# Kernel optimization log

Hardware: AMD Instinct MI355X
Metric: run time of the kernel (lower is better)

The kernel has to match this reference:

```python
import jax, jax.numpy as jnp
import numpy as np


def setup_inputs() -> dict:
    key = jax.random.key(0)
    # coeffs_tensor: stacked/padded wavelet coefficients [B, F, T]
    coeffs = jax.random.normal(key, (16, 256, 8192), dtype=jnp.float32)
    return {"coeffs": coeffs}


def reference(coeffs) -> jnp.ndarray:
    B, F, T = coeffs.shape
    # torch.angle on a real tensor -> 0 for x>=0, pi for x<0; jnp.angle matches.
    phase = jnp.angle(coeffs)
    inst_freq = jnp.diff(phase, axis=-1)
    inst_freq = jnp.pad(inst_freq, ((0, 0), (0, 0), (0, 1)))  # F.pad(..., (0,1))
    freq_adjusted = jnp.clip(inst_freq, -1.0, 1.0)  # [B,F,T]
    # k = (f + freq_adjusted).long(); .long() truncates toward zero, as does astype(int32)
    f_idx = jnp.arange(F, dtype=coeffs.dtype)[None, :, None]
    k = jnp.clip((f_idx + freq_adjusted).astype(jnp.int32), 0, F - 1)  # [B,F,T]
    # Fused scatter-add over all (b, f, t): sst[b, k[b,f,t], t] += coeffs[b, f, t]
    b_idx = jnp.arange(B)[:, None, None]
    t_idx = jnp.arange(T)[None, None, :]
    sst = jnp.zeros_like(coeffs).at[b_idx, k, t_idx].add(coeffs)
    return sst
```

## Files before the change

kernel.cpp:

```cpp
#include <hip/hip_runtime.h>

#define BB 16
#define FF 256
#define TT 8192
#define F_CHUNK 64
#define THREADS 256

__device__ __forceinline__ int sgn_bit(float x) {
    return (int)(__float_as_uint(x) >> 31);
}

__global__ __launch_bounds__(THREADS) void sst_kernel(const float* __restrict__ in,
                                                      float* __restrict__ out) {
    const int t   = blockIdx.x * (THREADS * 4) + threadIdx.x * 4;
    const int fs  = blockIdx.y * F_CHUNK;
    const int b   = blockIdx.z;
    const int lane = threadIdx.x & 63;

    const float* src = in  + (size_t)b * FF * TT + t;
    float*       dst = out + (size_t)b * FF * TT + t;

    const bool tail = (t + 4 >= TT);

    float4 vprev, vcur, vnext;
    int4   aprev, acur, anext;

    auto load_row = [&](int f, float4& v, int4& a) {
        v = *reinterpret_cast<const float4*>(src + (size_t)f * TT);
        float nxt = __shfl_down(v.x, 1, 64);
        if (lane == 63) {
            nxt = tail ? 0.0f : src[(size_t)f * TT + 4];
        }
        const int s0 = sgn_bit(v.x), s1 = sgn_bit(v.y), s2 = sgn_bit(v.z),
                  s3 = sgn_bit(v.w), s4 = sgn_bit(nxt);
        a.x = s1 - s0;
        a.y = s2 - s1;
        a.z = s3 - s2;
        a.w = tail ? 0 : (s4 - s3);
    };

    if (fs == 0) {
        aprev = make_int4(9, 9, 9, 9);
        vprev = make_float4(0.f, 0.f, 0.f, 0.f);
    } else {
        load_row(fs - 1, vprev, aprev);
    }
    load_row(fs, vcur, acur);

    #pragma unroll 4
    for (int g = fs; g < fs + F_CHUNK; ++g) {
        if (g + 1 < FF) {
            load_row(g + 1, vnext, anext);
        } else {
            anext = make_int4(9, 9, 9, 9);
            vnext = make_float4(0.f, 0.f, 0.f, 0.f);
        }

        const bool isFirst = (g == 0);
        const bool isLast  = (g == FF - 1);

        float4 r;
        {
            const bool bc = (acur.x == 0) || (isFirst && acur.x < 0) || (isLast && acur.x > 0);
            r.x = ((aprev.x == 1) ? vprev.x : 0.f) + (bc ? vcur.x : 0.f)
                + ((anext.x == -1) ? vnext.x : 0.f);
        }
        {
            const bool bc = (acur.y == 0) || (isFirst && acur.y < 0) || (isLast && acur.y > 0);
            r.y = ((aprev.y == 1) ? vprev.y : 0.f) + (bc ? vcur.y : 0.f)
                + ((anext.y == -1) ? vnext.y : 0.f);
        }
        {
            const bool bc = (acur.z == 0) || (isFirst && acur.z < 0) || (isLast && acur.z > 0);
            r.z = ((aprev.z == 1) ? vprev.z : 0.f) + (bc ? vcur.z : 0.f)
                + ((anext.z == -1) ? vnext.z : 0.f);
        }
        {
            const bool bc = (acur.w == 0) || (isFirst && acur.w < 0) || (isLast && acur.w > 0);
            r.w = ((aprev.w == 1) ? vprev.w : 0.f) + (bc ? vcur.w : 0.f)
                + ((anext.w == -1) ? vnext.w : 0.f);
        }

        *reinterpret_cast<float4*>(dst + (size_t)g * TT) = r;

        vprev = vcur; aprev = acur;
        vcur  = vnext; acur  = anext;
    }
}

extern "C" void kernel_launch(void* const* d_in, const int* in_sizes, int n_in,
                              void* d_out, int out_size, void* d_ws, size_t ws_size,
                              hipStream_t stream) {
    const float* in  = (const float*)d_in[0];
    float*       out = (float*)d_out;
    dim3 grid(TT / (THREADS * 4), FF / F_CHUNK, BB);
    sst_kernel<<<grid, THREADS, 0, stream>>>(in, out);
}
```

Before: 272.4 us.

## Prefetch rows two ahead and shrink frequency chunk for more blocks

Splits the row load into a raw-load step and a separate sign-difference step, so the load for row g+2 is issued before row g+1's data is consumed. This gives a software-pipelined prefetch that hides global memory latency. F_CHUNK also drops from 64 to 16, which quadruples the grid size for more parallelism and fully unrolls the loop. The cost is more halo rows loaded per block (about 18 rows read per 16 written) and higher register pressure.

```diff
diff --git a/kernel.cpp b/kernel.cpp
--- a/kernel.cpp
+++ b/kernel.cpp
@@ -3,18 +3,20 @@
 #define BB 16
 #define FF 256
 #define TT 8192
-#define F_CHUNK 64
+#define F_CHUNK 16
 #define THREADS 256
 
 __device__ __forceinline__ int sgn_bit(float x) {
     return (int)(__float_as_uint(x) >> 31);
 }
 
+struct Raw { float4 v; float e; };
+
 __global__ __launch_bounds__(THREADS) void sst_kernel(const float* __restrict__ in,
                                                       float* __restrict__ out) {
-    const int t   = blockIdx.x * (THREADS * 4) + threadIdx.x * 4;
-    const int fs  = blockIdx.y * F_CHUNK;
-    const int b   = blockIdx.z;
+    const int t    = blockIdx.x * (THREADS * 4) + threadIdx.x * 4;
+    const int fs   = blockIdx.y * F_CHUNK;
+    const int b    = blockIdx.z;
     const int lane = threadIdx.x & 63;
 
     const float* src = in  + (size_t)b * FF * TT + t;
@@ -22,35 +24,51 @@
 
     const bool tail = (t + 4 >= TT);
 
-    float4 vprev, vcur, vnext;
-    int4   aprev, acur, anext;
-
-    auto load_row = [&](int f, float4& v, int4& a) {
-        v = *reinterpret_cast<const float4*>(src + (size_t)f * TT);
-        float nxt = __shfl_down(v.x, 1, 64);
-        if (lane == 63) {
-            nxt = tail ? 0.0f : src[(size_t)f * TT + 4];
-        }
-        const int s0 = sgn_bit(v.x), s1 = sgn_bit(v.y), s2 = sgn_bit(v.z),
-                  s3 = sgn_bit(v.w), s4 = sgn_bit(nxt);
+    auto load_raw = [&](int f) {
+        Raw r;
+        r.v = *reinterpret_cast<const float4*>(src + (size_t)f * TT);
+        r.e = (lane == 63 && !tail) ? src[(size_t)f * TT + 4] : 0.0f;
+        return r;
+    };
+    auto adj_of = [&](const Raw& r) {
+        float nxt = __shfl_down(r.v.x, 1, 64);
+        if (lane == 63) nxt = r.e;
+        const int s0 = sgn_bit(r.v.x), s1 = sgn_bit(r.v.y), s2 = sgn_bit(r.v.z),
+                  s3 = sgn_bit(r.v.w), s4 = sgn_bit(nxt);
+        int4 a;
         a.x = s1 - s0;
         a.y = s2 - s1;
         a.z = s3 - s2;
         a.w = tail ? 0 : (s4 - s3);
+        return a;
     };
+
+    float4 vprev, vcur, vnext;
+    int4   aprev, acur, anext;
+    Raw    rn, rn2;
 
     if (fs == 0) {
         aprev = make_int4(9, 9, 9, 9);
         vprev = make_float4(0.f, 0.f, 0.f, 0.f);
     } else {
-        load_row(fs - 1, vprev, aprev);
+        Raw r = load_raw(fs - 1);
+        vprev = r.v; aprev = adj_of(r);
     }
-    load_row(fs, vcur, acur);
+    {
+        Raw r = load_raw(fs);
+        vcur = r.v; acur = adj_of(r);
+    }
+    rn = load_raw(fs + 1);
 
-    #pragma unroll 4
-    for (int g = fs; g < fs + F_CHUNK; ++g) {
+    #pragma unroll
+    for (int i = 0; i < F_CHUNK; ++i) {
+        const int g = fs + i;
+
+        const bool want2 = (i + 2 <= F_CHUNK) && (g + 2 < FF);
+        if (want2) rn2 = load_raw(g + 2);
+
         if (g + 1 < FF) {
-            load_row(g + 1, vnext, anext);
+            vnext = rn.v; anext = adj_of(rn);
         } else {
             anext = make_int4(9, 9, 9, 9);
             vnext = make_float4(0.f, 0.f, 0.f, 0.f);
@@ -83,8 +101,9 @@
 
         *reinterpret_cast<float4*>(dst + (size_t)g * TT) = r;
 
-        vprev = vcur; aprev = acur;
+        vprev = vcur;  aprev = acur;
         vcur  = vnext; acur  = anext;
+        rn    = rn2;
     }
 }
 
```

Result: faster. 240.9 us (-11.6%).
